# Kernel optimization log

Hardware: AMD Instinct MI355X
Metric: run time of the kernel (lower is better)

Reference implementation:

```python
import jax, jax.numpy as jnp
import numpy as np

DIM, VDIM, HEADS = 128, 384, 4
EPS_GN = 1e-5
EPS_RMS = 1.1920929e-7  # torch.finfo(float32).eps (nn.RMSNorm eps=None default)


def conv2d(x, w, pad):
    return jax.lax.conv_general_dilated(
        x, w, (1, 1), [(pad, pad), (pad, pad)],
        dimension_numbers=('NCHW', 'OIHW', 'NCHW'))


def group_norm(x, groups=8, eps=EPS_GN):
    b, c, h, w = x.shape
    xg = x.reshape(b, groups, -1)
    mu = xg.mean(-1, keepdims=True)
    var = jnp.mean((xg - mu) ** 2, -1, keepdims=True)
    return ((xg - mu) * jax.lax.rsqrt(var + eps)).reshape(b, c, h, w)


def rms_norm(x, w, eps=EPS_RMS):
    ms = jnp.mean(x * x, -1, keepdims=True)
    return x * jax.lax.rsqrt(ms + eps) * w


def enc_block(x, conv_w, proj_w=None):
    # encoder(): conv(k, bias=False) -> GroupNorm(8) -> SiLU, residual skip
    k = conv_w.shape[-1]
    y = jax.nn.silu(group_norm(conv2d(x, conv_w, k // 2)))
    skip = x if proj_w is None else conv2d(x, proj_w, 0)
    return y + skip


def rotate_half(x):
    x1, x2 = jnp.split(x, 2, -1)
    return jnp.concatenate([-x2, x1], -1)


def adaptive_avg_pool(x, oh, ow):
    b, c, h, w = x.shape  # h % oh == 0, w % ow == 0 here
    return x.reshape(b, c, oh, h // oh, ow, w // ow).mean((3, 5))


def create_coordinate(h, w):
    ys = (jnp.arange(h, dtype=jnp.float32) + 0.5) / h
    xs = (jnp.arange(w, dtype=jnp.float32) + 0.5) / w
    gy, gx = jnp.meshgrid(ys, xs, indexing='ij')
    return jnp.stack([gy, gx], -1).reshape(h * w, 2)  # (hw, 2)


def rope_freqs(dim=DIM, theta=100.0):
    f1 = theta ** jnp.linspace(0.0, -1.0, dim // 4)
    f1 = jnp.concatenate([f1, f1])  # (dim//2,)
    f2 = jnp.zeros((2, dim))
    f2 = f2.at[0, : dim // 2].set(f1)
    f2 = f2.at[1, dim // 2:].set(f1)
    return (f2 * 2.0 * np.pi).astype(jnp.float32)


def setup_inputs() -> dict:
    key = jax.random.key(0)
    ks = jax.random.split(key, 16)
    s = 0.05
    inp = {
        'image': jax.random.normal(ks[0], (4, 3, 224, 224), jnp.float32),
        'features': jax.random.normal(ks[1], (4, 384, 14, 14), jnp.float32),
        'rope_f': rope_freqs(),
        'img_conv_w': jax.random.normal(ks[2], (DIM, 3, 1, 1)) * s,
        'img_proj_w': jax.random.normal(ks[3], (DIM, 3, 1, 1)) * s,
        'qenc_w': jax.random.normal(ks[4], (DIM, DIM, 1, 1)) * s,
        'kenc_w': jax.random.normal(ks[5], (DIM, DIM, 1, 1)) * s,
        'kfeat_conv_w': jax.random.normal(ks[6], (DIM, VDIM, 1, 1)) * s,
        'kfeat_proj_w': jax.random.normal(ks[7], (DIM, VDIM, 1, 1)) * s,
        'sft_gamma_w': jax.random.normal(ks[8], (DIM, DIM, 1, 1)) * s,
        'sft_beta_w': jax.random.normal(ks[9], (DIM, DIM, 1, 1)) * s,
        'block_conv_w': jax.random.normal(ks[10], (DIM, DIM, 3, 3)) * s,
        'rms_q_w': jnp.ones((DIM,), jnp.float32),
        'rms_k_w': jnp.ones((DIM,), jnp.float32),
        'q_proj_w': jax.random.normal(ks[11], (DIM, DIM)) * s,
        'q_proj_b': jnp.zeros((DIM,), jnp.float32),
        'k_proj_w': jax.random.normal(ks[12], (DIM, DIM)) * s,
        'k_proj_b': jnp.zeros((DIM,), jnp.float32),
        'oh': 112,
        'ow': 112,
    }
    return inp


def jafar_forward(image, features, rope_f, img_conv_w, img_proj_w, qenc_w,
                  kenc_w, kfeat_conv_w, kfeat_proj_w, sft_gamma_w, sft_beta_w,
                  block_conv_w, rms_q_w, rms_k_w, q_proj_w, q_proj_b,
                  k_proj_w, k_proj_b, oh, ow):
    B = image.shape[0]
    # --- image encoder + RoPE over full-res tokens ---
    enc = enc_block(image, img_conv_w, img_proj_w)           # (B, dim, H, W)
    _, _, H, W = enc.shape
    coords = create_coordinate(H, W)                          # (HW, 2)
    tok = enc.reshape(B, DIM, H * W).transpose(0, 2, 1)       # (B, HW, dim)
    angle = coords @ rope_f                                   # (HW, dim)
    tok = tok * jnp.cos(angle) + rotate_half(tok) * jnp.sin(angle)
    enc = tok.transpose(0, 2, 1).reshape(B, DIM, H, W)

    # --- upsample ---
    fh, fw = features.shape[-2:]
    q = enc_block(enc, qenc_w)
    q = group_norm(adaptive_avg_pool(q, oh, ow))              # (B, dim, oh, ow)
    k = adaptive_avg_pool(enc_block(enc, kenc_w), fh, fw)     # (B, dim, fh, fw)
    fn = features * jax.lax.rsqrt(
        jnp.maximum(jnp.sum(features * features, 1, keepdims=True), 1e-24))
    kf = enc_block(fn, kfeat_conv_w, kfeat_proj_w)            # (B, dim, fh, fw)
    # SFT: gamma(kf) * GroupNorm(k) + beta(kf)
    k = conv2d(kf, sft_gamma_w, 0) * group_norm(k) + conv2d(kf, sft_beta_w, 0)

    # --- cross-attention block ---
    q = conv2d(q, block_conv_w, 1)                            # 3x3 conv on queries
    qt = q.reshape(B, DIM, oh * ow).transpose(0, 2, 1)        # (B, Nq, dim)
    kt = k.reshape(B, DIM, fh * fw).transpose(0, 2, 1)        # (B, Nk, dim)
    vt = features.reshape(B, VDIM, fh * fw).transpose(0, 2, 1)  # raw values

    qn = rms_norm(qt, rms_q_w)
    kn = rms_norm(kt, rms_k_w)
    hd = DIM // HEADS
    qp = (qn @ q_proj_w.T + q_proj_b).reshape(B, -1, HEADS, hd)
    kp = (kn @ k_proj_w.T + k_proj_b).reshape(B, -1, HEADS, hd)
    scores = jnp.einsum('bqhd,bkhd->bhqk', qp, kp) / np.sqrt(hd)
    attn = jax.nn.softmax(scores, -1).mean(1)                 # head-avg (B,Nq,Nk)
    out = jnp.einsum('bij,bjd->bid', attn, vt)                # vs RAW values
    return out.transpose(0, 2, 1).reshape(B, VDIM, oh, ow)


def reference(image, features, rope_f, img_conv_w, img_proj_w, qenc_w, kenc_w,
              kfeat_conv_w, kfeat_proj_w, sft_gamma_w, sft_beta_w, block_conv_w,
              rms_q_w, rms_k_w, q_proj_w, q_proj_b, k_proj_w, k_proj_b, oh, ow):
    return jafar_forward(image, features, rope_f, img_conv_w, img_proj_w,
                         qenc_w, kenc_w, kfeat_conv_w, kfeat_proj_w,
                         sft_gamma_w, sft_beta_w, block_conv_w, rms_q_w,
                         rms_k_w, q_proj_w, q_proj_b, k_proj_w, k_proj_b,
                         oh, ow)
```

## Files before the change

kernel.cpp:

```cpp
#include <hip/hip_runtime.h>
#include <cstdint>
#include <cstddef>

#define DEV __device__ __forceinline__

namespace {

constexpr int BB   = 4;
constexpr int HWP  = 50176;
constexpr int NQ   = 12544;
constexpr int NKk  = 196;
constexpr int VD   = 384;
constexpr float EPS_GN  = 1e-5f;
constexpr float EPS_RMS = 1.1920929e-7f;

typedef __attribute__((ext_vector_type(4))) float f32x4;
typedef __attribute__((ext_vector_type(4))) _Float16 h16x4;
typedef __attribute__((ext_vector_type(8))) _Float16 h16x8;

DEV float silu_f(float z) { return z / (1.f + __expf(-z)); }
DEV int rfl(int v) { return __builtin_amdgcn_readfirstlane(v); }

DEV f32x4 mfma16(h16x4 a, h16x4 b, f32x4 c) {
  return __builtin_amdgcn_mfma_f32_16x16x16f16(a, b, c, 0, 0, 0);
}
DEV f32x4 mfma32(h16x8 a, h16x8 b, f32x4 c) {
  return __builtin_amdgcn_mfma_f32_16x16x32_f16(a, b, c, 0, 0, 0);
}

DEV void pack16_one(int id, const float* W, const float* rowscale,
                    _Float16* dst) {
  int j = id & 3, l = (id >> 2) & 63, tile = id >> 8;
  int ct = tile & 7, kt = tile >> 3;
  int ci = kt * 16 + 4 * (l >> 4) + j;
  int co = ct * 16 + (l & 15);
  float v = W[(size_t)co * 128 + ci];
  if (rowscale) v *= rowscale[ci];
  dst[id] = (_Float16)v;
}
DEV void pack32_one(int id, const float* W, _Float16* dst) {
  int j = id & 7, l = (id >> 3) & 63, ct = (id >> 9) & 7, kt2 = id >> 12;
  int u = l >> 4;
  int ci = kt2 * 32 + ((j < 4) ? (4 * u + j) : (16 + 4 * u + (j - 4)));
  int co = ct * 16 + (l & 15);
  dst[id] = (_Float16)W[(size_t)co * 128 + ci];
}
DEV void pack384_one(int id, const float* W, _Float16* dst) {
  int j = id & 3, l = (id >> 2) & 63, rest = id >> 8;
  int ct = rest & 7, kt = rest >> 3;
  int ci = kt * 16 + 4 * (l >> 4) + j;
  int co = ct * 16 + (l & 15);
  dst[id] = (_Float16)W[(size_t)co * 384 + ci];
}

__global__ __launch_bounds__(256) void k_prep(
    const float* __restrict__ qenc_w, const float* __restrict__ kenc_w,
    const float* __restrict__ q_proj_w, const float* __restrict__ rms_q_w,
    const float* __restrict__ block_conv_w,
    const float* __restrict__ kfeat_conv_w, const float* __restrict__ kfeat_proj_w,
    const float* __restrict__ sft_gamma_w, const float* __restrict__ sft_beta_w,
    const float* __restrict__ k_proj_w, const float* __restrict__ rms_k_w,
    const float* __restrict__ ropef, const float* __restrict__ feat,
    _Float16* __restrict__ WqB, _Float16* __restrict__ WkB,
    _Float16* __restrict__ QPB, _Float16* __restrict__ W3B,
    _Float16* __restrict__ KFB, _Float16* __restrict__ KFPB,
    _Float16* __restrict__ GB, _Float16* __restrict__ BBf,
    _Float16* __restrict__ KPB,
    float* __restrict__ cosT, float* __restrict__ sinT,
    _Float16* __restrict__ featB) {
  int idx = blockIdx.x * 256 + threadIdx.x;
  if (idx < 16384) {
    pack32_one(idx, qenc_w, WqB);
  } else if (idx < 32768) {
    pack32_one(idx - 16384, kenc_w, WkB);
  } else if (idx < 49152) {
    pack16_one(idx - 32768, q_proj_w, rms_q_w, QPB);
  } else if (idx < 196608) {
    int id = idx - 49152;
    int j = id & 7, l = (id >> 3) & 63, ct = (id >> 9) & 7;
    int kt2 = (id >> 12) & 3, tap = id >> 14;
    int ci = kt2 * 32 + 8 * (l >> 4) + j;
    int co = ct * 16 + (l & 15);
    W3B[id] = (_Float16)block_conv_w[((size_t)co * 128 + ci) * 9 + tap];
  } else if (idx < 245760) {
    pack384_one(idx - 196608, kfeat_conv_w, KFB);
  } else if (idx < 294912) {
    pack384_one(idx - 245760, kfeat_proj_w, KFPB);
  } else if (idx < 311296) {
    pack16_one(idx - 294912, sft_gamma_w, nullptr, GB);
  } else if (idx < 327680) {
    pack16_one(idx - 311296, sft_beta_w, nullptr, BBf);
  } else if (idx < 344064) {
    pack16_one(idx - 327680, k_proj_w, rms_k_w, KPB);
  } else if (idx < 358400) {
    int id = idx - 344064;
    int pos = id >> 6, d = id & 63;
    float a = (pos + 0.5f) * (1.f / 224.f) * ropef[d];
    float s, c;
    __sincosf(a, &s, &c);
    cosT[id] = c;
    sinT[id] = s;
  } else if (idx < 677888) {
    int id = idx - 358400;
    int j = id & 3, l = (id >> 2) & 63;
    int rest = id >> 8;
    int dt = rest % 24;
    int kt = (rest / 24) % 13;
    int b = rest / (24 * 13);
    int key = kt * 16 + 4 * (l >> 4) + j;
    int d = dt * 16 + (l & 15);
    float v = (key < 196) ? feat[((size_t)(b * 384) + d) * 196 + key] : 0.f;
    featB[id] = (_Float16)v;
  }
}


__global__ __launch_bounds__(256) void k_imgstat1(
    const float* __restrict__ img, float* __restrict__ part) {
  __shared__ float lds[4][9];
  int b = blockIdx.x >> 6, blk = blockIdx.x & 63;
  int t = threadIdx.x;
  float a[9];
#pragma unroll
  for (int j = 0; j < 9; ++j) a[j] = 0.f;
  const float* ib = img + (size_t)b * 3 * HWP;
  for (int pix = blk * 784 + t; pix < blk * 784 + 784; pix += 256) {
    float x0 = ib[pix], x1 = ib[HWP + pix], x2 = ib[2 * HWP + pix];
    a[0] += x0; a[1] += x1; a[2] += x2;
    a[3] += x0 * x0; a[4] += x0 * x1; a[5] += x0 * x2;
    a[6] += x1 * x1; a[7] += x1 * x2; a[8] += x2 * x2;
  }
#pragma unroll
  for (int j = 0; j < 9; ++j)
    for (int m = 1; m < 64; m <<= 1) a[j] += __shfl_xor(a[j], m);
  if ((t & 63) == 0)
    for (int j = 0; j < 9; ++j) lds[t >> 6][j] = a[j];
  __syncthreads();
  if (t < 9)
    part[(size_t)blockIdx.x * 9 + t] =
        lds[0][t] + lds[1][t] + lds[2][t] + lds[3][t];
}

__global__ __launch_bounds__(128) void k_imgstat2(
    const float* __restrict__ part, const float* __restrict__ wimg,
    float* __restrict__ img_murs) {
  __shared__ float MG[9];
  int b = blockIdx.x, t = threadIdx.x;
  if (t < 9) {
    float s = 0.f;
    for (int i = 0; i < 64; ++i) s += part[(size_t)(b * 64 + i) * 9 + t];
    MG[t] = s;
  }
  __syncthreads();
  int c = t;
  float w0 = wimg[c * 3], w1 = wimg[c * 3 + 1], w2 = wimg[c * 3 + 2];
  float s1 = w0 * MG[0] + w1 * MG[1] + w2 * MG[2];
  float s2 = w0 * w0 * MG[3] + w1 * w1 * MG[6] + w2 * w2 * MG[8] +
             2.f * (w0 * w1 * MG[4] + w0 * w2 * MG[5] + w1 * w2 * MG[7]);
  for (int m = 1; m < 16; m <<= 1) {
    s1 += __shfl_xor(s1, m);
    s2 += __shfl_xor(s2, m);
  }
  if ((c & 15) == 0) {
    int g = c >> 4;
    float invN = 1.f / (16.f * HWP);
    float mu = s1 * invN;
    float var = s2 * invN - mu * mu;
    img_murs[b * 16 + g] = mu;
    img_murs[b * 16 + 8 + g] = rsqrtf(var + EPS_GN);
  }
}


__global__ __launch_bounds__(256) void k_gram(
    const float* __restrict__ img, const float* __restrict__ cosT,
    const float* __restrict__ sinT,
    const float* __restrict__ wimg, const float* __restrict__ wimgp,
    const float* __restrict__ img_murs,
    _Float16* __restrict__ encF,
    float* __restrict__ Gpart, float* __restrict__ mpart) {
  __shared__ __align__(16) _Float16 fragP[2080 * 4];
  __shared__ __align__(16) _Float16 fragC[8192];
  __shared__ float sWc[384], sWp[384], sMu[8], sRs[8];
  int t = threadIdx.x, l = t & 63, w = t >> 6;
  int b = blockIdx.x / 98, blk = blockIdx.x % 98;
  for (int i = t; i < 384; i += 256) { sWc[i] = wimg[i]; sWp[i] = wimgp[i]; }
  if (t < 8) { sMu[t] = img_murs[b * 16 + t]; sRs[t] = img_murs[b * 16 + 8 + t]; }
  f32x4 acc[2][8];
  f32x4 macc[2];
  f32x4 z = {0.f, 0.f, 0.f, 0.f};
#pragma unroll
  for (int e = 0; e < 2; ++e) {
    macc[e] = z;
#pragma unroll
    for (int nt = 0; nt < 8; ++nt) acc[e][nt] = z;
  }
  h16x4 hone = {(_Float16)1.f, (_Float16)1.f, (_Float16)1.f, (_Float16)1.f};
  int mt = l >> 4;
  int laneCbase = 16 * ((l & 15) >> 2);
  int jC = (l & 15) & 3;
  for (int s = 0; s < 8; ++s) {
    int sub = blk * 8 + s;
    int tile = sub >> 2, st = sub & 3;
    int py = (tile / 14) * 16 + ((st >> 1) << 3) + (l >> 3);
    int px = (tile % 14) * 16 + ((st & 1) << 3) + (l & 7);
    __syncthreads();
    {
      const float* ip = img + (size_t)b * 3 * HWP + py * 224 + px;
      float x0 = ip[0], x1 = ip[HWP], x2 = ip[2 * HWP];
      const float* cy = cosT + py * 64 + w * 16;
      const float* sy = sinT + py * 64 + w * 16;
      const float* cx = cosT + px * 64 + w * 16;
      const float* sx = sinT + px * 64 + w * 16;
#pragma unroll
      for (int jj = 0; jj < 4; ++jj) {
        f32x4 cyv = *(const f32x4*)(cy + jj * 4);
        f32x4 syv = *(const f32x4*)(sy + jj * 4);
        f32x4 cxv = *(const f32x4*)(cx + jj * 4);
        f32x4 sxv = *(const f32x4*)(sx + jj * 4);
        h16x4 lo4, hi4;
#pragma unroll
        for (int u = 0; u < 4; ++u) {
          int d = w * 16 + jj * 4 + u;
          int c2 = d + 64;
          float y1 = sWc[d * 3] * x0 + sWc[d * 3 + 1] * x1 + sWc[d * 3 + 2] * x2;
          float s1 = sWp[d * 3] * x0 + sWp[d * 3 + 1] * x1 + sWp[d * 3 + 2] * x2;
          float y2 = sWc[c2 * 3] * x0 + sWc[c2 * 3 + 1] * x1 + sWc[c2 * 3 + 2] * x2;
          float s2 = sWp[c2 * 3] * x0 + sWp[c2 * 3 + 1] * x1 + sWp[c2 * 3 + 2] * x2;
          int g1 = d >> 4, g2 = g1 + 4;
          float t1 = silu_f((y1 - sMu[g1]) * sRs[g1]) + s1;
          float t2 = silu_f((y2 - sMu[g2]) * sRs[g2]) + s2;
          lo4[u] = (_Float16)(t1 * cyv[u] - t2 * syv[u]);
          hi4[u] = (_Float16)(t2 * cxv[u] + t1 * sxv[u]);
        }
        int lane = (l & 15) + 16 * jj;
        *(h16x4*)&fragP[((w * 4 + mt) * 65 + lane) * 4]       = lo4;
        *(h16x4*)&fragP[(((w + 4) * 4 + mt) * 65 + lane) * 4] = hi4;
#pragma unroll
        for (int u = 0; u < 4; ++u) {
          int laneC = jj * 4 + u + laneCbase;
          fragC[((mt * 8 + w) * 64 + laneC) * 4 + jC]     = lo4[u];
          fragC[((mt * 8 + w + 4) * 64 + laneC) * 4 + jC] = hi4[u];
        }
      }
    }
    __syncthreads();
    _Float16* ef = encF + ((size_t)(b * 784) + sub) * 8192;
    for (int i = t; i < 1024; i += 256) {
      int kt2 = i >> 8, m2 = (i >> 6) & 3, ln = i & 63;
      h16x4 lo = *(const h16x4*)&fragP[(((2 * kt2) * 4 + m2) * 65 + ln) * 4];
      h16x4 hi = *(const h16x4*)&fragP[(((2 * kt2 + 1) * 4 + m2) * 65 + ln) * 4];
      h16x8 v;
#pragma unroll
      for (int j = 0; j < 4; ++j) { v[j] = lo[j]; v[j + 4] = hi[j]; }
      *(h16x8*)(ef + (size_t)i * 8) = v;
    }
#pragma unroll
    for (int pk = 0; pk < 4; ++pk) {
      h16x4 a0 = *(const h16x4*)&fragC[((pk * 8 + 2 * w) * 64 + l) * 4];
      h16x4 a1 = *(const h16x4*)&fragC[((pk * 8 + 2 * w + 1) * 64 + l) * 4];
      macc[0] = mfma16(a0, hone, macc[0]);
      macc[1] = mfma16(a1, hone, macc[1]);
#pragma unroll
      for (int nt = 0; nt < 8; ++nt) {
        h16x4 bv = *(const h16x4*)&fragC[((pk * 8 + nt) * 64 + l) * 4];
        acc[0][nt] = mfma16(a0, bv, acc[0][nt]);
        acc[1][nt] = mfma16(a1, bv, acc[1][nt]);
      }
    }
  }
  float* gp = Gpart + (size_t)(b * 98 + blk) * 16384;
#pragma unroll
  for (int e = 0; e < 2; ++e)
#pragma unroll
    for (int nt = 0; nt < 8; ++nt)
#pragma unroll
      for (int r = 0; r < 4; ++r) {
        int row = (2 * w + e) * 16 + 4 * (l >> 4) + r;
        int col = nt * 16 + (l & 15);
        gp[row * 128 + col] = acc[e][nt][r];
      }
  if ((l & 15) == 0) {
    float* mp = mpart + (size_t)(b * 98 + blk) * 128;
#pragma unroll
    for (int e = 0; e < 2; ++e)
#pragma unroll
      for (int r = 0; r < 4; ++r)
        mp[(2 * w + e) * 16 + 4 * (l >> 4) + r] = macc[e][r];
  }
}

__global__ void k_gred(const float* __restrict__ Gpart,
                       const float* __restrict__ mpart,
                       float* __restrict__ G, float* __restrict__ mvec) {
  int b = blockIdx.x >> 6, chunk = blockIdx.x & 63;
  int idx = chunk * 256 + threadIdx.x;
  float s = 0.f;
  for (int i = 0; i < 98; ++i) s += Gpart[(size_t)(b * 98 + i) * 16384 + idx];
  G[(size_t)b * 16384 + idx] = s;
  if (idx < 128) {
    float sm = 0.f;
    for (int i = 0; i < 98; ++i) sm += mpart[(size_t)(b * 98 + i) * 128 + idx];
    mvec[b * 128 + idx] = sm;
  }
}

__global__ __launch_bounds__(256) void k_gstats(
    const float* __restrict__ G, const float* __restrict__ mvec,
    const float* __restrict__ qw, const float* __restrict__ kw,
    float* __restrict__ qk_murs) {
  __shared__ float red1[4], red2[4];
  int bi = blockIdx.x;
  int conv = bi >> 5, b = (bi >> 3) & 3, g = bi & 7;
  const float* W = conv ? kw : qw;
  int t = threadIdx.x;
  int c = g * 16 + (t >> 4);
  int i0 = (t & 15) * 8;
  const float* wc = W + (size_t)c * 128;
  const float* Gb = G + (size_t)b * 16384;
  const float* mb = mvec + b * 128;
  float s1 = 0.f, s2 = 0.f;
  for (int i = i0; i < i0 + 8; ++i) {
    float gi = 0.f;
    for (int j = 0; j < 128; ++j) gi += Gb[i * 128 + j] * wc[j];
    s2 += wc[i] * gi;
    s1 += wc[i] * mb[i];
  }
  for (int m = 1; m < 64; m <<= 1) { s1 += __shfl_xor(s1, m); s2 += __shfl_xor(s2, m); }
  if ((t & 63) == 0) { red1[t >> 6] = s1; red2[t >> 6] = s2; }
  __syncthreads();
  if (t == 0) {
    float S1 = red1[0] + red1[1] + red1[2] + red1[3];
    float S2 = red2[0] + red2[1] + red2[2] + red2[3];
    float invN = 1.f / 802816.f;
    float mu = S1 * invN;
    float var = S2 * invN - mu * mu;
    qk_murs[bi * 2] = mu;
    qk_murs[bi * 2 + 1] = rsqrtf(var + EPS_GN);
  }
}


__global__ __launch_bounds__(256) void k_passA2(
    const _Float16* __restrict__ encF, const float* __restrict__ qk_murs,
    const _Float16* __restrict__ WqB, const _Float16* __restrict__ WkB,
    float* __restrict__ q_pool, float* __restrict__ kpp,
    float* __restrict__ Qpart) {
  int t = threadIdx.x, l = t & 63;
  int wu = rfl(t >> 6);
  int bi = blockIdx.x;
  int b = bi / 784, sub = bi % 784;
  int tile = sub >> 2, st = sub & 3;
  int by = (tile / 14) * 16, bx = (tile % 14) * 16;
  float qmu[2], qrs[2], kmu[2], krs[2];
#pragma unroll
  for (int cc = 0; cc < 2; ++cc) {
    int g = 2 * wu + cc;
    qmu[cc] = qk_murs[(b * 8 + g) * 2];
    qrs[cc] = qk_murs[(b * 8 + g) * 2 + 1];
    kmu[cc] = qk_murs[(32 + b * 8 + g) * 2];
    krs[cc] = qk_murs[(32 + b * 8 + g) * 2 + 1];
  }
  const h16x8* EF = (const h16x8*)encF + ((size_t)(b * 784) + sub) * 1024;
  const h16x8* WQ = (const h16x8*)WqB;
  const h16x8* WK = (const h16x8*)WkB;
  f32x4 z = {0.f, 0.f, 0.f, 0.f};
  f32x4 accQ[4][2], accK[4][2];
  h16x8 sf8[4];
#pragma unroll
  for (int mt = 0; mt < 4; ++mt)
#pragma unroll
    for (int cc = 0; cc < 2; ++cc) { accQ[mt][cc] = z; accK[mt][cc] = z; }
  for (int kt2 = 0; kt2 < 4; ++kt2) {
    h16x8 a[4];
#pragma unroll
    for (int mt = 0; mt < 4; ++mt) a[mt] = EF[(kt2 * 4 + mt) * 64 + l];
    if (kt2 == wu) {
#pragma unroll
      for (int mt = 0; mt < 4; ++mt) sf8[mt] = a[mt];
    }
    int fi = (kt2 * 8 + 2 * wu) * 64 + l;
    h16x8 bq0 = WQ[fi];
    h16x8 bq1 = WQ[fi + 64];
    h16x8 bk0 = WK[fi];
    h16x8 bk1 = WK[fi + 64];
#pragma unroll
    for (int mt = 0; mt < 4; ++mt) {
      accQ[mt][0] = mfma32(bq0, a[mt], accQ[mt][0]);
      accQ[mt][1] = mfma32(bq1, a[mt], accQ[mt][1]);
      accK[mt][0] = mfma32(bk0, a[mt], accK[mt][0]);
      accK[mt][1] = mfma32(bk1, a[mt], accK[mt][1]);
    }
  }
  int q = l & 15;
  bool act = (q & 9) == 0;
  float kacc[2][4];
  float qs1[2] = {0.f, 0.f}, qs2[2] = {0.f, 0.f};
#pragma unroll
  for (int cc = 0; cc < 2; ++cc)
#pragma unroll
    for (int r = 0; r < 4; ++r) kacc[cc][r] = 0.f;
#pragma unroll
  for (int cc = 0; cc < 2; ++cc) {
    int g = 2 * wu + cc;
#pragma unroll
    for (int mt = 0; mt < 4; ++mt) {
      f32x4 pv;
#pragma unroll
      for (int r = 0; r < 4; ++r) {
        float skip = (float)sf8[mt][cc * 4 + r];
        pv[r] = silu_f((accQ[mt][cc][r] - qmu[cc]) * qrs[cc]) + skip;
        kacc[cc][r] += silu_f((accK[mt][cc][r] - kmu[cc]) * krs[cc]) + skip;
      }
#pragma unroll
      for (int r = 0; r < 4; ++r) {
        float v = pv[r] + __shfl_xor(pv[r], 1);
        v += __shfl_xor(v, 8);
        pv[r] = v * 0.25f;
      }
      if (act) {
        int p = mt * 16 + q;
        int py = by + (st >> 1) * 8 + (p >> 3);
        int px = bx + (st & 1) * 8 + (p & 7);
        size_t base = ((size_t)(b * NQ) + (py >> 1) * 112 + (px >> 1)) * 128 +
                      g * 16 + 4 * (l >> 4);
        *(f32x4*)(q_pool + base) = pv;
        qs1[cc] += pv[0] + pv[1] + pv[2] + pv[3];
        qs2[cc] += pv[0] * pv[0] + pv[1] * pv[1] + pv[2] * pv[2] + pv[3] * pv[3];
      }
    }
  }
#pragma unroll
  for (int cc = 0; cc < 2; ++cc) {
#pragma unroll
    for (int r = 0; r < 4; ++r) {
      float v = kacc[cc][r];
      v += __shfl_xor(v, 1);
      v += __shfl_xor(v, 2);
      v += __shfl_xor(v, 4);
      v += __shfl_xor(v, 8);
      kacc[cc][r] = v;
    }
    if (q == 0) {
      f32x4 kv = {kacc[cc][0], kacc[cc][1], kacc[cc][2], kacc[cc][3]};
      *(f32x4*)(kpp + (size_t)bi * 128 + (2 * wu + cc) * 16 + 4 * (l >> 4)) = kv;
    }
  }
#pragma unroll
  for (int cc = 0; cc < 2; ++cc) {
    float a1 = qs1[cc], a2 = qs2[cc];
    for (int m = 1; m < 64; m <<= 1) {
      a1 += __shfl_xor(a1, m);
      a2 += __shfl_xor(a2, m);
    }
    if (l == 0) {
      Qpart[(size_t)bi * 16 + (2 * wu + cc) * 2] = a1;
      Qpart[(size_t)bi * 16 + (2 * wu + cc) * 2 + 1] = a2;
    }
  }
}

__global__ __launch_bounds__(256) void k_kpred(
    const float* __restrict__ kpp, float* __restrict__ k_pool) {
  int idx = blockIdx.x * 256 + threadIdx.x;
  if (idx >= BB * 128 * NKk) return;
  int b = idx / (128 * NKk);
  int rem = idx % (128 * NKk);
  int c = rem / NKk, tile = rem % NKk;
  const float* base = kpp + ((size_t)(b * 196 + tile) * 4) * 128 + c;
  float s = base[0] + base[128] + base[256] + base[384];
  k_pool[idx] = s * (1.f / 256.f);
}

__global__ __launch_bounds__(256) void k_qstatfin(
    const float* __restrict__ Qpart, float* __restrict__ murs2) {
  __shared__ float l1[4], l2[4];
  int b = blockIdx.x >> 3, g = blockIdx.x & 7, t = threadIdx.x;
  float s1 = 0.f, s2 = 0.f;
  for (int i = t; i < 784; i += 256) {
    s1 += Qpart[((size_t)(b * 784) + i) * 16 + g * 2];
    s2 += Qpart[((size_t)(b * 784) + i) * 16 + g * 2 + 1];
  }
  for (int m = 1; m < 64; m <<= 1) { s1 += __shfl_xor(s1, m); s2 += __shfl_xor(s2, m); }
  if ((t & 63) == 0) { l1[t >> 6] = s1; l2[t >> 6] = s2; }
  __syncthreads();
  if (t == 0) {
    float a = l1[0] + l1[1] + l1[2] + l1[3];
    float bq = l2[0] + l2[1] + l2[2] + l2[3];
    float invN = 1.f / (16.f * (float)NQ);
    float mu = a * invN;
    float var = bq * invN - mu * mu;
    murs2[blockIdx.x * 2] = mu;
    murs2[blockIdx.x * 2 + 1] = rsqrtf(var + EPS_GN);
  }
}


__global__ __launch_bounds__(256) void k_gnstats(
    const float* __restrict__ src, float* __restrict__ murs, int P, float eps) {
  __shared__ float l1[4], l2[4];
  int b = blockIdx.x >> 3, g = blockIdx.x & 7, t = threadIdx.x;
  const float* base = src + ((size_t)(b * 128) + g * 16) * P;
  float s1 = 0.f, s2 = 0.f;
  for (int i = t; i < 16 * P; i += 256) {
    float v = base[i];
    s1 += v; s2 += v * v;
  }
  for (int m = 1; m < 64; m <<= 1) { s1 += __shfl_xor(s1, m); s2 += __shfl_xor(s2, m); }
  if ((t & 63) == 0) { l1[t >> 6] = s1; l2[t >> 6] = s2; }
  __syncthreads();
  if (t == 0) {
    float invN = 1.f / (16.f * (float)P);
    float a = l1[0] + l1[1] + l1[2] + l1[3];
    float bq = l2[0] + l2[1] + l2[2] + l2[3];
    float mu = a * invN;
    float var = bq * invN - mu * mu;
    murs[blockIdx.x * 2] = mu;
    murs[blockIdx.x * 2 + 1] = rsqrtf(var + eps);
  }
}


__global__ __launch_bounds__(256) void k_kf(
    const float* __restrict__ feat,
    const _Float16* __restrict__ KFB, const _Float16* __restrict__ KFPB,
    float* __restrict__ y_kf, float* __restrict__ skip_kf) {
  __shared__ __align__(16) _Float16 fnF[24 * 4 * 64 * 4];
  __shared__ float ssqL[4][64];
  __shared__ float rsqL[64];
  int t = threadIdx.x, l = t & 63, w = t >> 6;
  int b = blockIdx.x >> 2, tile = blockIdx.x & 3;
  int p0 = tile * 49;
  const float* fb = feat + (size_t)b * VD * NKk;
  {
    float s = 0.f;
    if (l < 49) {
#pragma unroll 4
      for (int k = w; k < VD; k += 4) {
        float v = fb[(size_t)k * NKk + p0 + l];
        s += v * v;
      }
    }
    ssqL[w][l] = s;
  }
  __syncthreads();
  if (t < 64) {
    float s = ssqL[0][t] + ssqL[1][t] + ssqL[2][t] + ssqL[3][t];
    rsqL[t] = rsqrtf(fmaxf(s, 1e-24f));
  }
  __syncthreads();
  for (int i = t; i < VD * 64; i += 256) {
    int k = i >> 6, p = i & 63;
    float v = 0.f;
    if (p < 49) v = fb[(size_t)k * NKk + p0 + p] * rsqL[p];
    int kt = k >> 4, kr = k & 15, u = kr >> 2, j = kr & 3, mt = p >> 4;
    fnF[(((kt * 4 + mt) * 64) + (p & 15) + 16 * u) * 4 + j] = (_Float16)v;
  }
  __syncthreads();
  f32x4 z = {0.f, 0.f, 0.f, 0.f};
  f32x4 accY[4][2], accS[4][2];
#pragma unroll
  for (int mt = 0; mt < 4; ++mt)
#pragma unroll
    for (int cc = 0; cc < 2; ++cc) { accY[mt][cc] = z; accS[mt][cc] = z; }
  for (int kt = 0; kt < 24; ++kt) {
    h16x4 a[4];
#pragma unroll
    for (int mt = 0; mt < 4; ++mt)
      a[mt] = *(const h16x4*)&fnF[((kt * 4 + mt) * 64 + l) * 4];
    int fi = (kt * 8 + 2 * w) * 64 + l;
    h16x4 by0 = *(const h16x4*)(KFB + (size_t)fi * 4);
    h16x4 by1 = *(const h16x4*)(KFB + (size_t)(fi + 64) * 4);
    h16x4 bs0 = *(const h16x4*)(KFPB + (size_t)fi * 4);
    h16x4 bs1 = *(const h16x4*)(KFPB + (size_t)(fi + 64) * 4);
#pragma unroll
    for (int mt = 0; mt < 4; ++mt) {
      accY[mt][0] = mfma16(a[mt], by0, accY[mt][0]);
      accY[mt][1] = mfma16(a[mt], by1, accY[mt][1]);
      accS[mt][0] = mfma16(a[mt], bs0, accS[mt][0]);
      accS[mt][1] = mfma16(a[mt], bs1, accS[mt][1]);
    }
  }
#pragma unroll
  for (int cc = 0; cc < 2; ++cc) {
    int co = (2 * w + cc) * 16 + (l & 15);
#pragma unroll
    for (int mt = 0; mt < 4; ++mt)
#pragma unroll
      for (int r = 0; r < 4; ++r) {
        int pix = mt * 16 + 4 * (l >> 4) + r;
        if (pix < 49) {
          size_t off = ((size_t)(b * 128) + co) * NKk + p0 + pix;
          y_kf[off] = accY[mt][cc][r];
          skip_kf[off] = accS[mt][cc][r];
        }
      }
  }
}


__global__ __launch_bounds__(256) void k_ksft(
    const float* __restrict__ y_kf, const float* __restrict__ skip_kf,
    const float* __restrict__ kf_murs, const float* __restrict__ kgn_murs,
    const _Float16* __restrict__ GB, const _Float16* __restrict__ BBf,
    const _Float16* __restrict__ KPB,
    const float* __restrict__ k_pool, const float* __restrict__ k_proj_b,
    float* __restrict__ kpb) {
  __shared__ __align__(16) _Float16 kfF[8 * 4 * 64 * 4];
  __shared__ float msL[4][64];
  __shared__ float sMu[8], sRs[8], sGmu[8], sGrs[8];
  int t = threadIdx.x, l = t & 63, w = t >> 6;
  int b = blockIdx.x >> 2, tile = blockIdx.x & 3;
  int p0 = tile * 49;
  if (t < 8) {
    sMu[t] = kf_murs[(b * 8 + t) * 2];
    sRs[t] = kf_murs[(b * 8 + t) * 2 + 1];
    sGmu[t] = kgn_murs[(b * 8 + t) * 2];
    sGrs[t] = kgn_murs[(b * 8 + t) * 2 + 1];
  }
  __syncthreads();
  for (int i = t; i < 128 * 64; i += 256) {
    int c = i >> 6, p = i & 63;
    float v = 0.f;
    if (p < 49) {
      size_t off = ((size_t)(b * 128) + c) * NKk + p0 + p;
      int g = c >> 4;
      v = silu_f((y_kf[off] - sMu[g]) * sRs[g]) + skip_kf[off];
    }
    int kt = c >> 4, kr = c & 15, u = kr >> 2, j = kr & 3, mt = p >> 4;
    kfF[(((kt * 4 + mt) * 64) + (p & 15) + 16 * u) * 4 + j] = (_Float16)v;
  }
  __syncthreads();
  f32x4 z = {0.f, 0.f, 0.f, 0.f};
  f32x4 accG[4][2], accB[4][2];
#pragma unroll
  for (int mt = 0; mt < 4; ++mt)
#pragma unroll
    for (int cc = 0; cc < 2; ++cc) { accG[mt][cc] = z; accB[mt][cc] = z; }
  for (int kt = 0; kt < 8; ++kt) {
    h16x4 a[4];
#pragma unroll
    for (int mt = 0; mt < 4; ++mt)
      a[mt] = *(const h16x4*)&kfF[((kt * 4 + mt) * 64 + l) * 4];
    int fi = (kt * 8 + 2 * w) * 64 + l;
    h16x4 bg0 = *(const h16x4*)(GB + (size_t)fi * 4);
    h16x4 bg1 = *(const h16x4*)(GB + (size_t)(fi + 64) * 4);
    h16x4 bb0 = *(const h16x4*)(BBf + (size_t)fi * 4);
    h16x4 bb1 = *(const h16x4*)(BBf + (size_t)(fi + 64) * 4);
#pragma unroll
    for (int mt = 0; mt < 4; ++mt) {
      accG[mt][0] = mfma16(a[mt], bg0, accG[mt][0]);
      accG[mt][1] = mfma16(a[mt], bg1, accG[mt][1]);
      accB[mt][0] = mfma16(a[mt], bb0, accB[mt][0]);
      accB[mt][1] = mfma16(a[mt], bb1, accB[mt][1]);
    }
  }
  float kfin[4][2][4];
#pragma unroll
  for (int cc = 0; cc < 2; ++cc) {
    int g = 2 * w + cc;
    int co = g * 16 + (l & 15);
    float gmu = sGmu[g], grs = sGrs[g];
#pragma unroll
    for (int mt = 0; mt < 4; ++mt)
#pragma unroll
      for (int r = 0; r < 4; ++r) {
        int pix = mt * 16 + 4 * (l >> 4) + r;
        float v = 0.f;
        if (pix < 49) {
          float kn = (k_pool[((size_t)(b * 128) + co) * NKk + p0 + pix] - gmu) * grs;
          v = fmaf(accG[mt][cc][r], kn, accB[mt][cc][r]);
        }
        kfin[mt][cc][r] = v;
      }
  }
#pragma unroll
  for (int mt = 0; mt < 4; ++mt)
#pragma unroll
    for (int r = 0; r < 4; ++r) {
      float s2 = kfin[mt][0][r] * kfin[mt][0][r] + kfin[mt][1][r] * kfin[mt][1][r];
      for (int m = 1; m < 16; m <<= 1) s2 += __shfl_xor(s2, m);
      if ((l & 15) == 0) msL[w][mt * 16 + 4 * (l >> 4) + r] = s2;
    }
  __syncthreads();
#pragma unroll
  for (int cc = 0; cc < 2; ++cc) {
    int ktn = 2 * w + cc;
    int u = (l & 15) >> 2, j = (l & 15) & 3;
#pragma unroll
    for (int mt = 0; mt < 4; ++mt)
#pragma unroll
      for (int r = 0; r < 4; ++r) {
        int lane = (4 * (l >> 4) + r) + 16 * u;
        kfF[((ktn * 4 + mt) * 64 + lane) * 4 + j] = (_Float16)kfin[mt][cc][r];
      }
  }
  __syncthreads();
  f32x4 accP[4][2];
#pragma unroll
  for (int mt = 0; mt < 4; ++mt)
#pragma unroll
    for (int cc = 0; cc < 2; ++cc) accP[mt][cc] = z;
  for (int kt = 0; kt < 8; ++kt) {
    h16x4 a[4];
#pragma unroll
    for (int mt = 0; mt < 4; ++mt)
      a[mt] = *(const h16x4*)&kfF[((kt * 4 + mt) * 64 + l) * 4];
    int fi = (kt * 8 + 2 * w) * 64 + l;
    h16x4 b0 = *(const h16x4*)(KPB + (size_t)fi * 4);
    h16x4 b1 = *(const h16x4*)(KPB + (size_t)(fi + 64) * 4);
#pragma unroll
    for (int mt = 0; mt < 4; ++mt) {
      accP[mt][0] = mfma16(a[mt], b0, accP[mt][0]);
      accP[mt][1] = mfma16(a[mt], b1, accP[mt][1]);
    }
  }
#pragma unroll
  for (int mt = 0; mt < 4; ++mt)
#pragma unroll
    for (int r = 0; r < 4; ++r) {
      int pix = mt * 16 + 4 * (l >> 4) + r;
      if (pix >= 49) continue;
      float ms = msL[0][pix] + msL[1][pix] + msL[2][pix] + msL[3][pix];
      float rr = rsqrtf(ms * (1.f / 128.f) + EPS_RMS);
#pragma unroll
      for (int cc = 0; cc < 2; ++cc) {
        int co = (2 * w + cc) * 16 + (l & 15);
        kpb[((size_t)(b * 196) + p0 + pix) * 128 + co] =
            accP[mt][cc][r] * rr + k_proj_b[co];
      }
    }
}


__global__ __launch_bounds__(256) void k_conv3f(
    const float* __restrict__ q_pool, const float* __restrict__ murs2,
    const _Float16* __restrict__ W3B, const _Float16* __restrict__ QPB,
    const float* __restrict__ bias, float* __restrict__ qp) {
  __shared__ __align__(16) _Float16 tileL[100 * 136];
  __shared__ float sMu[8], sRs[8];
  int t = threadIdx.x, l = t & 63, w = t >> 6;
  int b = blockIdx.x / 196, reg = blockIdx.x % 196;
  int y0 = (reg / 14) * 8, x0 = (reg % 14) * 8;
  if (t < 8) { sMu[t] = murs2[(b * 8 + t) * 2]; sRs[t] = murs2[(b * 8 + t) * 2 + 1]; }
  __syncthreads();
  for (int i = t; i < 3200; i += 256) {
    int rowp = i >> 5, c4 = i & 31;
    int gy = y0 - 1 + rowp / 10, gx = x0 - 1 + rowp % 10;
    h16x4 hv = {(_Float16)0.f, (_Float16)0.f, (_Float16)0.f, (_Float16)0.f};
    if (gy >= 0 && gy < 112 && gx >= 0 && gx < 112) {
      f32x4 v = *(const f32x4*)(q_pool + ((size_t)(b * NQ) + gy * 112 + gx) * 128 +
                                c4 * 4);
      int g = c4 >> 2;
      float mu = sMu[g], rs = sRs[g];
#pragma unroll
      for (int j = 0; j < 4; ++j) hv[j] = (_Float16)((v[j] - mu) * rs);
    }
    *(h16x4*)&tileL[rowp * 136 + c4 * 4] = hv;
  }
  __syncthreads();
  f32x4 z = {0.f, 0.f, 0.f, 0.f};
  f32x4 acc[8];
#pragma unroll
  for (int ct = 0; ct < 8; ++ct) acc[ct] = z;
  int lm = l & 15;
  int mrow = lm >> 3, mcol = lm & 7;
  const h16x8* W3l = (const h16x8*)W3B + l;
  h16x8 wbuf[3][8];
#pragma unroll
  for (int ct = 0; ct < 8; ++ct) wbuf[0][ct] = W3l[ct * 64];
#pragma unroll
  for (int ct = 0; ct < 8; ++ct) wbuf[1][ct] = W3l[(8 + ct) * 64];
#pragma unroll
  for (int s = 0; s < 36; ++s) {
    if (s + 2 < 36) {
#pragma unroll
      for (int ct = 0; ct < 8; ++ct)
        wbuf[(s + 2) % 3][ct] = W3l[((s + 2) * 8 + ct) * 64];
    }
    int tap = s >> 2, kt2 = s & 3;
    int prow = (2 * w + mrow + tap / 3) * 10 + (mcol + tap % 3);
    h16x8 bf = *(const h16x8*)&tileL[prow * 136 + kt2 * 32 + 8 * (l >> 4)];
#pragma unroll
    for (int ct = 0; ct < 8; ++ct)
      acc[ct] = mfma32(wbuf[s % 3][ct], bf, acc[ct]);
  }
  float sq = 0.f;
#pragma unroll
  for (int ct = 0; ct < 8; ++ct)
#pragma unroll
    for (int r = 0; r < 4; ++r) sq += acc[ct][r] * acc[ct][r];
  sq += __shfl_xor(sq, 16);
  sq += __shfl_xor(sq, 32);
  float rr = rsqrtf(sq * (1.f / 128.f) + EPS_RMS);
  int chof = 4 * (l >> 4);
  h16x4 pb[8];
#pragma unroll
  for (int kt = 0; kt < 8; ++kt)
#pragma unroll
    for (int j = 0; j < 4; ++j) pb[kt][j] = (_Float16)acc[kt][j];
  f32x4 accP[8];
#pragma unroll
  for (int ct = 0; ct < 8; ++ct) accP[ct] = z;
  const h16x4* QP = (const h16x4*)QPB + l;
#pragma unroll
  for (int kt = 0; kt < 8; ++kt) {
#pragma unroll
    for (int ct = 0; ct < 8; ++ct)
      accP[ct] = mfma16(QP[(kt * 8 + ct) * 64], pb[kt], accP[ct]);
  }
  int py = y0 + 2 * w + mrow, px = x0 + mcol;
  size_t pbase = ((size_t)(b * NQ) + py * 112 + px) * 128;
#pragma unroll
  for (int ct = 0; ct < 8; ++ct) {
    f32x4 o;
#pragma unroll
    for (int r = 0; r < 4; ++r)
      o[r] = accP[ct][r] * rr + bias[ct * 16 + chof + r];
    *(f32x4*)(qp + pbase + ct * 16 + chof) = o;
  }
}


__global__ __launch_bounds__(256) void k_attn1m(
    const float* __restrict__ qp, const float* __restrict__ kpb,
    _Float16* __restrict__ Ph) {
  __shared__ float sP[4][16][212];
  int t = threadIdx.x, l = t & 63, h = t >> 6;
  int b = blockIdx.x / 784, qt = blockIdx.x % 784;
  int q0 = qt * 16;
  constexpr float SC = 0.17677669529663687f;
  h16x8 aq;
  {
    const float* qrow = qp + ((size_t)(b * NQ) + q0 + (l & 15)) * 128 +
                        h * 32 + 8 * (l >> 4);
    f32x4 v0 = *(const f32x4*)qrow;
    f32x4 v1 = *(const f32x4*)(qrow + 4);
#pragma unroll
    for (int j = 0; j < 4; ++j) { aq[j] = (_Float16)v0[j]; aq[j + 4] = (_Float16)v1[j]; }
  }
  f32x4 z = {0.f, 0.f, 0.f, 0.f};
  f32x4 acc[13];
#pragma unroll
  for (int nt = 0; nt < 13; ++nt) acc[nt] = z;
#pragma unroll
  for (int nt = 0; nt < 13; ++nt) {
    int key = nt * 16 + (l & 15);
    bool ok = key < 196;
    h16x8 bf = {(_Float16)0.f, (_Float16)0.f, (_Float16)0.f, (_Float16)0.f,
                (_Float16)0.f, (_Float16)0.f, (_Float16)0.f, (_Float16)0.f};
    if (ok) {
      const float* krow = kpb + ((size_t)(b * 196) + key) * 128 +
                          h * 32 + 8 * (l >> 4);
      f32x4 v0 = *(const f32x4*)krow;
      f32x4 v1 = *(const f32x4*)(krow + 4);
#pragma unroll
      for (int j = 0; j < 4; ++j) { bf[j] = (_Float16)v0[j]; bf[j + 4] = (_Float16)v1[j]; }
    }
    acc[nt] = mfma32(aq, bf, acc[nt]);
  }
#pragma unroll
  for (int r = 0; r < 4; ++r) {
    float mx = -3e38f;
#pragma unroll
    for (int nt = 0; nt < 13; ++nt) {
      bool ok = nt * 16 + (l & 15) < 196;
      float v = ok ? acc[nt][r] * SC : -3e38f;
      acc[nt][r] = v;
      mx = fmaxf(mx, v);
    }
    for (int m = 1; m < 16; m <<= 1) mx = fmaxf(mx, __shfl_xor(mx, m));
    float sum = 0.f;
#pragma unroll
    for (int nt = 0; nt < 13; ++nt) {
      bool ok = nt * 16 + (l & 15) < 196;
      float e = ok ? __expf(acc[nt][r] - mx) : 0.f;
      acc[nt][r] = e;
      sum += e;
    }
    for (int m = 1; m < 16; m <<= 1) sum += __shfl_xor(sum, m);
    float inv = 1.f / sum;
#pragma unroll
    for (int nt = 0; nt < 13; ++nt)
      sP[h][4 * (l >> 4) + r][nt * 16 + (l & 15)] = acc[nt][r] * inv;
  }
  __syncthreads();
  _Float16* pb = Ph + (size_t)(b * 784 + qt) * 13 * 256;
  for (int i = t; i < 832; i += 256) {
    int kt = i >> 6, ll = i & 63;
    int q = ll & 15, kb = kt * 16 + 4 * (ll >> 4);
    h16x4 v;
#pragma unroll
    for (int j = 0; j < 4; ++j) {
      int k = kb + j;
      float s = 0.25f * (sP[0][q][k] + sP[1][q][k] + sP[2][q][k] + sP[3][q][k]);
      v[j] = (_Float16)s;
    }
    *(h16x4*)(pb + (size_t)i * 4) = v;
  }
}


__global__ __launch_bounds__(256) void k_attn2m(
    const _Float16* __restrict__ Ph, const _Float16* __restrict__ featB,
    float* __restrict__ out) {
  int t = threadIdx.x, l = t & 63, w = t >> 6;
  int b = blockIdx.x / 196, qt = blockIdx.x % 196;
  int q16 = qt * 4 + w;
  f32x4 z = {0.f, 0.f, 0.f, 0.f};
  f32x4 acc[24];
#pragma unroll
  for (int dt = 0; dt < 24; ++dt) acc[dt] = z;
  const h16x4* PB = (const h16x4*)Ph + ((size_t)(b * 784 + q16) * 13) * 64 + l;
  const h16x4* FB = (const h16x4*)featB + (size_t)b * 13 * 24 * 64 + l;
  for (int kt = 0; kt < 13; ++kt) {
    h16x4 bp = PB[kt * 64];
    const h16x4* fb = FB + kt * 24 * 64;
#pragma unroll
    for (int dt = 0; dt < 24; ++dt)
      acc[dt] = mfma16(fb[(size_t)dt * 64], bp, acc[dt]);
  }
  int qg = q16 * 16 + (l & 15);
#pragma unroll
  for (int dt = 0; dt < 24; ++dt)
#pragma unroll
    for (int r = 0; r < 4; ++r) {
      int d = dt * 16 + 4 * (l >> 4) + r;
      out[((size_t)(b * 384) + d) * NQ + qg] = acc[dt][r];
    }
}

}

extern "C" void kernel_launch(void* const* d_in, const int* in_sizes, int n_in,
                              void* d_out, int out_size, void* d_ws,
                              size_t ws_size, hipStream_t stream) {
  (void)in_sizes; (void)n_in; (void)out_size; (void)ws_size;
  const float* image        = (const float*)d_in[0];
  const float* features     = (const float*)d_in[1];
  const float* rope_f       = (const float*)d_in[2];
  const float* img_conv_w   = (const float*)d_in[3];
  const float* img_proj_w   = (const float*)d_in[4];
  const float* qenc_w       = (const float*)d_in[5];
  const float* kenc_w       = (const float*)d_in[6];
  const float* kfeat_conv_w = (const float*)d_in[7];
  const float* kfeat_proj_w = (const float*)d_in[8];
  const float* sft_gamma_w  = (const float*)d_in[9];
  const float* sft_beta_w   = (const float*)d_in[10];
  const float* block_conv_w = (const float*)d_in[11];
  const float* rms_q_w      = (const float*)d_in[12];
  const float* rms_k_w      = (const float*)d_in[13];
  const float* q_proj_w     = (const float*)d_in[14];
  const float* q_proj_b     = (const float*)d_in[15];
  const float* k_proj_w     = (const float*)d_in[16];
  const float* k_proj_b     = (const float*)d_in[17];
  float* out = (float*)d_out;
  float* ws = (float*)d_ws;

  size_t off = 0;
  auto alloc = [&](size_t n) {
    size_t r = off;
    off += (n + 63) & ~(size_t)63;
    return r;
  };
  _Float16* WqB  = (_Float16*)(ws + alloc(8192));
  _Float16* WkB  = (_Float16*)(ws + alloc(8192));
  _Float16* QPB  = (_Float16*)(ws + alloc(8192));
  _Float16* W3B  = (_Float16*)(ws + alloc(73728));
  _Float16* KFB  = (_Float16*)(ws + alloc(24576));
  _Float16* KFPB = (_Float16*)(ws + alloc(24576));
  _Float16* GB   = (_Float16*)(ws + alloc(8192));
  _Float16* BBf  = (_Float16*)(ws + alloc(8192));
  _Float16* KPB  = (_Float16*)(ws + alloc(8192));
  float* cosT     = ws + alloc(14336);
  float* sinT     = ws + alloc(14336);
  _Float16* featB = (_Float16*)(ws + alloc(159744));
  float* imgpart  = ws + alloc(2304);
  float* img_murs = ws + alloc(64);
  float* qk_murs  = ws + alloc(128);
  float* murs2    = ws + alloc(64);
  float* kgn_murs = ws + alloc(64);
  float* kf_murs  = ws + alloc(64);
  float* G        = ws + alloc(65536);
  float* mvec     = ws + alloc(512);
  float* mpart    = ws + alloc(392 * 128);
  float* Qpart    = ws + alloc((size_t)BB * 784 * 16);
  float* kpp      = ws + alloc((size_t)BB * 784 * 128);
  float* y_kf     = ws + alloc(100352);
  float* skip_kf  = ws + alloc(100352);
  float* k_pool   = ws + alloc(100352);
  float* kpb      = ws + alloc(100352);
  float* RA = ws + alloc((size_t)BB * NQ * 128);
  float* ENCp = ws + alloc((size_t)BB * 784 * 8192 / 2);
  float* Gpart  = RA;
  float* q_pool = RA;
  _Float16* encF = (_Float16*)ENCp;
  float* qp      = ENCp;
  _Float16* Ph   = (_Float16*)(ENCp + (size_t)BB * NQ * 128);

  k_prep<<<2648, 256, 0, stream>>>(qenc_w, kenc_w, q_proj_w, rms_q_w,
                                   block_conv_w, kfeat_conv_w, kfeat_proj_w,
                                   sft_gamma_w, sft_beta_w, k_proj_w, rms_k_w,
                                   rope_f, features,
                                   WqB, WkB, QPB, W3B, KFB, KFPB, GB, BBf, KPB,
                                   cosT, sinT, featB);

  k_imgstat1<<<BB * 64, 256, 0, stream>>>(image, imgpart);
  k_imgstat2<<<BB, 128, 0, stream>>>(imgpart, img_conv_w, img_murs);

  k_kf<<<BB * 4, 256, 0, stream>>>(features, KFB, KFPB, y_kf, skip_kf);
  k_gnstats<<<32, 256, 0, stream>>>(y_kf, kf_murs, NKk, EPS_GN);

  k_gram<<<BB * 98, 256, 0, stream>>>(image, cosT, sinT, img_conv_w,
                                      img_proj_w, img_murs, encF, Gpart, mpart);
  k_gred<<<BB * 64, 256, 0, stream>>>(Gpart, mpart, G, mvec);
  k_gstats<<<64, 256, 0, stream>>>(G, mvec, qenc_w, kenc_w, qk_murs);

  k_passA2<<<BB * 784, 256, 0, stream>>>(encF, qk_murs, WqB, WkB,
                                         q_pool, kpp, Qpart);
  k_qstatfin<<<32, 256, 0, stream>>>(Qpart, murs2);
  k_kpred<<<392, 256, 0, stream>>>(kpp, k_pool);
  k_gnstats<<<32, 256, 0, stream>>>(k_pool, kgn_murs, NKk, EPS_GN);

  k_ksft<<<BB * 4, 256, 0, stream>>>(y_kf, skip_kf, kf_murs, kgn_murs,
                                     GB, BBf, KPB, k_pool, k_proj_b, kpb);

  k_conv3f<<<BB * 196, 256, 0, stream>>>(q_pool, murs2, W3B, QPB, q_proj_b, qp);

  k_attn1m<<<BB * 784, 256, 0, stream>>>(qp, kpb, Ph);
  k_attn2m<<<BB * 196, 256, 0, stream>>>(Ph, featB, out);
}
```

Measured before the change: 390.1 us.

## Split fused Q/K encoder pass into separate kernels and use fast reciprocal in SiLU

The combined pass that computed both the Q and K encoder GEMMs per tile is split into two kernels, k_passK and k_passQ. Each one holds half the accumulators, so register pressure drops and occupancy can rise. In exchange the encF tile is read twice and there is one extra launch. SiLU also swaps a true division for the hardware reciprocal approximation, which is slightly less precise.

```diff
diff --git a/kernel.cpp b/kernel.cpp
--- a/kernel.cpp
+++ b/kernel.cpp
@@ -18,7 +18,9 @@
 typedef __attribute__((ext_vector_type(4))) _Float16 h16x4;
 typedef __attribute__((ext_vector_type(8))) _Float16 h16x8;
 
-DEV float silu_f(float z) { return z / (1.f + __expf(-z)); }
+DEV float silu_f(float z) {
+  return z * __builtin_amdgcn_rcpf(1.f + __expf(-z));
+}
 DEV int rfl(int v) { return __builtin_amdgcn_readfirstlane(v); }
 
 DEV f32x4 mfma16(h16x4 a, h16x4 b, f32x4 c) {
@@ -341,36 +343,32 @@
 }
 
 
-__global__ __launch_bounds__(256) void k_passA2(
+__global__ __launch_bounds__(256) void k_passQ(
     const _Float16* __restrict__ encF, const float* __restrict__ qk_murs,
-    const _Float16* __restrict__ WqB, const _Float16* __restrict__ WkB,
-    float* __restrict__ q_pool, float* __restrict__ kpp,
-    float* __restrict__ Qpart) {
+    const _Float16* __restrict__ WqB,
+    float* __restrict__ q_pool, float* __restrict__ Qpart) {
   int t = threadIdx.x, l = t & 63;
   int wu = rfl(t >> 6);
   int bi = blockIdx.x;
   int b = bi / 784, sub = bi % 784;
   int tile = sub >> 2, st = sub & 3;
   int by = (tile / 14) * 16, bx = (tile % 14) * 16;
-  float qmu[2], qrs[2], kmu[2], krs[2];
+  float qmu[2], qrs[2];
 #pragma unroll
   for (int cc = 0; cc < 2; ++cc) {
     int g = 2 * wu + cc;
     qmu[cc] = qk_murs[(b * 8 + g) * 2];
     qrs[cc] = qk_murs[(b * 8 + g) * 2 + 1];
-    kmu[cc] = qk_murs[(32 + b * 8 + g) * 2];
-    krs[cc] = qk_murs[(32 + b * 8 + g) * 2 + 1];
   }
   const h16x8* EF = (const h16x8*)encF + ((size_t)(b * 784) + sub) * 1024;
   const h16x8* WQ = (const h16x8*)WqB;
-  const h16x8* WK = (const h16x8*)WkB;
   f32x4 z = {0.f, 0.f, 0.f, 0.f};
-  f32x4 accQ[4][2], accK[4][2];
+  f32x4 accQ[4][2];
   h16x8 sf8[4];
 #pragma unroll
   for (int mt = 0; mt < 4; ++mt)
 #pragma unroll
-    for (int cc = 0; cc < 2; ++cc) { accQ[mt][cc] = z; accK[mt][cc] = z; }
+    for (int cc = 0; cc < 2; ++cc) accQ[mt][cc] = z;
   for (int kt2 = 0; kt2 < 4; ++kt2) {
     h16x8 a[4];
 #pragma unroll
@@ -382,24 +380,15 @@
     int fi = (kt2 * 8 + 2 * wu) * 64 + l;
     h16x8 bq0 = WQ[fi];
     h16x8 bq1 = WQ[fi + 64];
-    h16x8 bk0 = WK[fi];
-    h16x8 bk1 = WK[fi + 64];
 #pragma unroll
     for (int mt = 0; mt < 4; ++mt) {
       accQ[mt][0] = mfma32(bq0, a[mt], accQ[mt][0]);
       accQ[mt][1] = mfma32(bq1, a[mt], accQ[mt][1]);
-      accK[mt][0] = mfma32(bk0, a[mt], accK[mt][0]);
-      accK[mt][1] = mfma32(bk1, a[mt], accK[mt][1]);
     }
   }
   int q = l & 15;
   bool act = (q & 9) == 0;
-  float kacc[2][4];
   float qs1[2] = {0.f, 0.f}, qs2[2] = {0.f, 0.f};
-#pragma unroll
-  for (int cc = 0; cc < 2; ++cc)
-#pragma unroll
-    for (int r = 0; r < 4; ++r) kacc[cc][r] = 0.f;
 #pragma unroll
   for (int cc = 0; cc < 2; ++cc) {
     int g = 2 * wu + cc;
@@ -410,7 +399,6 @@
       for (int r = 0; r < 4; ++r) {
         float skip = (float)sf8[mt][cc * 4 + r];
         pv[r] = silu_f((accQ[mt][cc][r] - qmu[cc]) * qrs[cc]) + skip;
-        kacc[cc][r] += silu_f((accK[mt][cc][r] - kmu[cc]) * krs[cc]) + skip;
       }
 #pragma unroll
       for (int r = 0; r < 4; ++r) {
@@ -432,6 +420,78 @@
   }
 #pragma unroll
   for (int cc = 0; cc < 2; ++cc) {
+    float a1 = qs1[cc], a2 = qs2[cc];
+    for (int m = 1; m < 64; m <<= 1) {
+      a1 += __shfl_xor(a1, m);
+      a2 += __shfl_xor(a2, m);
+    }
+    if (l == 0) {
+      Qpart[(size_t)bi * 16 + (2 * wu + cc) * 2] = a1;
+      Qpart[(size_t)bi * 16 + (2 * wu + cc) * 2 + 1] = a2;
+    }
+  }
+}
+
+
+__global__ __launch_bounds__(256) void k_passK(
+    const _Float16* __restrict__ encF, const float* __restrict__ qk_murs,
+    const _Float16* __restrict__ WkB, float* __restrict__ kpp) {
+  int t = threadIdx.x, l = t & 63;
+  int wu = rfl(t >> 6);
+  int bi = blockIdx.x;
+  int b = bi / 784, sub = bi % 784;
+  float kmu[2], krs[2];
+#pragma unroll
+  for (int cc = 0; cc < 2; ++cc) {
+    int g = 2 * wu + cc;
+    kmu[cc] = qk_murs[(32 + b * 8 + g) * 2];
+    krs[cc] = qk_murs[(32 + b * 8 + g) * 2 + 1];
+  }
+  const h16x8* EF = (const h16x8*)encF + ((size_t)(b * 784) + sub) * 1024;
+  const h16x8* WK = (const h16x8*)WkB;
+  f32x4 z = {0.f, 0.f, 0.f, 0.f};
+  f32x4 accK[4][2];
+  h16x8 sf8[4];
+#pragma unroll
+  for (int mt = 0; mt < 4; ++mt)
+#pragma unroll
+    for (int cc = 0; cc < 2; ++cc) accK[mt][cc] = z;
+  for (int kt2 = 0; kt2 < 4; ++kt2) {
+    h16x8 a[4];
+#pragma unroll
+    for (int mt = 0; mt < 4; ++mt) a[mt] = EF[(kt2 * 4 + mt) * 64 + l];
+    if (kt2 == wu) {
+#pragma unroll
+      for (int mt = 0; mt < 4; ++mt) sf8[mt] = a[mt];
+    }
+    int fi = (kt2 * 8 + 2 * wu) * 64 + l;
+    h16x8 bk0 = WK[fi];
+    h16x8 bk1 = WK[fi + 64];
+#pragma unroll
+    for (int mt = 0; mt < 4; ++mt) {
+      accK[mt][0] = mfma32(bk0, a[mt], accK[mt][0]);
+      accK[mt][1] = mfma32(bk1, a[mt], accK[mt][1]);
+    }
+  }
+  int q = l & 15;
+  float kacc[2][4];
+#pragma unroll
+  for (int cc = 0; cc < 2; ++cc)
+#pragma unroll
+    for (int r = 0; r < 4; ++r) kacc[cc][r] = 0.f;
+#pragma unroll
+  for (int cc = 0; cc < 2; ++cc) {
+#pragma unroll
+    for (int mt = 0; mt < 4; ++mt) {
+#pragma unroll
+      for (int r = 0; r < 4; ++r) {
+        float skip = (float)sf8[mt][cc * 4 + r];
+        kacc[cc][r] += silu_f((accK[mt][cc][r] - kmu[cc]) * krs[cc]) + skip;
+      }
+    }
+  }
+#pragma unroll
+  for (int cc = 0; cc < 2; ++cc) {
 #pragma unroll
     for (int r = 0; r < 4; ++r) {
       float v = kacc[cc][r];
@@ -444,18 +504,6 @@
     if (q == 0) {
       f32x4 kv = {kacc[cc][0], kacc[cc][1], kacc[cc][2], kacc[cc][3]};
       *(f32x4*)(kpp + (size_t)bi * 128 + (2 * wu + cc) * 16 + 4 * (l >> 4)) = kv;
-    }
-  }
-#pragma unroll
-  for (int cc = 0; cc < 2; ++cc) {
-    float a1 = qs1[cc], a2 = qs2[cc];
-    for (int m = 1; m < 64; m <<= 1) {
-      a1 += __shfl_xor(a1, m);
-      a2 += __shfl_xor(a2, m);
-    }
-    if (l == 0) {
-      Qpart[(size_t)bi * 16 + (2 * wu + cc) * 2] = a1;
-      Qpart[(size_t)bi * 16 + (2 * wu + cc) * 2 + 1] = a2;
     }
   }
 }
@@ -1016,8 +1064,8 @@
   k_gred<<<BB * 64, 256, 0, stream>>>(Gpart, mpart, G, mvec);
   k_gstats<<<64, 256, 0, stream>>>(G, mvec, qenc_w, kenc_w, qk_murs);
 
-  k_passA2<<<BB * 784, 256, 0, stream>>>(encF, qk_murs, WqB, WkB,
-                                         q_pool, kpp, Qpart);
+  k_passK<<<BB * 784, 256, 0, stream>>>(encF, qk_murs, WkB, kpp);
+  k_passQ<<<BB * 784, 256, 0, stream>>>(encF, qk_murs, WqB, q_pool, Qpart);
   k_qstatfin<<<32, 256, 0, stream>>>(Qpart, murs2);
   k_kpred<<<392, 256, 0, stream>>>(kpp, k_pool);
   k_gnstats<<<32, 256, 0, stream>>>(k_pool, kgn_murs, NKk, EPS_GN);
```

Result: faster. 369.5 us (-5.3%).
